# Kernel tuning notes

Measured on AMD Instinct MI355X. Metric: run time of the kernel, lower is better.

The kernel has to match this reference:

```python
import jax, jax.numpy as jnp
import numpy as np

B, I, H = 32768, 128, 128


def setup_inputs() -> dict:
    key = jax.random.key(0)
    ks = jax.random.split(key, 11)
    s = 1.0 / np.sqrt(H)
    return {
        "x": jax.random.normal(ks[0], (B, I), jnp.float32),
        "h": jax.random.normal(ks[1], (B, H), jnp.float32),
        "c": jax.random.normal(ks[2], (B, H), jnp.float32),
        "W1": jax.random.normal(ks[3], (H, I + H), jnp.float32) * s,
        "b1": jax.random.normal(ks[4], (H,), jnp.float32) * s + 1.0,  # forget-gate bias offset 1.0
        "W2": jax.random.normal(ks[5], (H, I + H), jnp.float32) * s,
        "b2": jax.random.normal(ks[6], (H,), jnp.float32) * s,
        "Wf": jax.random.normal(ks[7], (H, I + H), jnp.float32) * s,
        "bf": jax.random.normal(ks[8], (H,), jnp.float32) * s,
        "W3": jax.random.normal(ks[9], (H, I + H), jnp.float32) * s,
        "b3": jax.random.normal(ks[10], (H,), jnp.float32) * s,
    }


def reference(x, h, c, W1, b1, W2, b2, Wf, bf, W3, b3):
    # total_in = inp + hidden (coordinate-list concat == feature concat)
    total = jnp.concatenate([x, h], axis=-1)  # [B, I+H]
    sig1 = jax.nn.sigmoid(total @ W1.T + b1)  # forget gate (bias offset +1)
    sig2 = jax.nn.sigmoid(total @ W2.T + b2)  # input gate
    f_l = jnp.tanh(total @ Wf.T + bf)         # candidate via symmetric f
    sig3 = jax.nn.sigmoid(total @ W3.T + b3)  # output gate
    new_c = c * sig1 + sig2 * f_l             # fused elementwise combine
    new_h = jnp.tanh(new_c) * sig3
    return new_h, new_c
```

## Files before the change

### kernel.cpp

```cpp
#include <hip/hip_runtime.h>

#define B_TOTAL 32768
#define NROWB   128
#define TILE    16
#define NT      8

typedef __attribute__((ext_vector_type(8)))  short    bf16x8;
typedef __attribute__((ext_vector_type(4)))  float    f32x4;
typedef __attribute__((ext_vector_type(2)))  unsigned u32x2;
typedef __attribute__((ext_vector_type(4)))  unsigned u32x4;

__device__ __forceinline__ unsigned rne1(float f) {
    unsigned u = __builtin_bit_cast(unsigned, f);
    return (u + 0x7FFFu + ((u >> 16) & 1u)) >> 16;
}
__device__ __forceinline__ unsigned cvtpk(float lo, float hi) {
    unsigned r;
    asm("v_cvt_pk_bf16_f32 %0, %1, %2" : "=v"(r) : "v"(lo), "v"(hi));
    return r;
}
__device__ __forceinline__ float fsig(float v) {
    return __fdividef(1.0f, 1.0f + __expf(-v));
}
__device__ __forceinline__ float ftanh(float v) {
    return 1.0f - __fdividef(2.0f, 1.0f + __expf(2.0f * v));
}

__global__ void wconv_kernel(const float* __restrict__ w1, const float* __restrict__ w2,
                             const float* __restrict__ wf, const float* __restrict__ w3,
                             u32x4* __restrict__ out) {
    int T = blockIdx.x * 256 + threadIdx.x;
    int F = T >> 6, l = T & 63;
    int s = F >> 4, tau = (F >> 3) & 1, ks = F & 7;
    int n16 = l & 15;
    int g = n16 & 3, hl = n16 >> 2;
    const float* W = (g == 0) ? w1 : (g == 1) ? w2 : (g == 2) ? wf : w3;
    const float* src = W + (s * 8 + tau * 4 + hl) * 256 + ks * 32 + (l >> 4) * 8;
    f32x4 lo = *(const f32x4*)src;
    f32x4 hi = *(const f32x4*)(src + 4);
    u32x4 r;
    r[0] = rne1(lo[0]) | (rne1(lo[1]) << 16);
    r[1] = rne1(lo[2]) | (rne1(lo[3]) << 16);
    r[2] = rne1(hi[0]) | (rne1(hi[1]) << 16);
    r[3] = rne1(hi[2]) | (rne1(hi[3]) << 16);
    out[T] = r;
}

__global__ __launch_bounds__(1024, 4) void lstm_kernel(
    const float* __restrict__ x, const float* __restrict__ h, const float* __restrict__ c,
    const bf16x8* __restrict__ wfrag,
    const float* __restrict__ b1, const float* __restrict__ b2,
    const float* __restrict__ bfv, const float* __restrict__ b3,
    float* __restrict__ out)
{
    __shared__ __align__(16) char smem[2][8192];

    const int tid  = threadIdx.x;
    const int wave = tid >> 6;
    const int lane = tid & 63;
    const int rb   = lane & 15;
    const int c4   = lane >> 4;
    const long row0 = (long)blockIdx.x * NROWB;
    const int col0 = wave * 8 + c4;
    const int col1 = col0 + 4;

    const int ksst  = lane & 7;
    const int chunk = lane >> 3;
    const int k0    = ksst * 32 + chunk * 4;
    const int stoff = ksst * 1024
        + (((((chunk >> 1) << 4) | wave) + ksst) & 63) * 16
        + (chunk & 1) * 8;

    f32x4 ar;
    auto A_ISSUE = [&](int t) {
        const float* base = (k0 < 128)
            ? (x + (row0 + (long)t * TILE + wave) * 128 + k0)
            : (h + (row0 + (long)t * TILE + wave) * 128 + (k0 - 128));
        ar = *(const f32x4*)base;
    };
    auto A_STORE = [&](int b) {
        u32x2 w;
        w[0] = cvtpk(ar[0], ar[1]);
        w[1] = cvtpk(ar[2], ar[3]);
        *(u32x2*)(smem[b & 1] + stoff) = w;
    };

    A_ISSUE(0);

    bf16x8 wfr[2][8];
#pragma unroll
    for (int tau = 0; tau < 2; ++tau)
#pragma unroll
        for (int ks = 0; ks < 8; ++ks)
            wfr[tau][ks] = wfrag[(size_t)((wave * 2 + tau) * 8 + ks) * 64 + lane];

    const f32x4 bias0 = (f32x4){ b1[col0], b2[col0], bfv[col0], b3[col0] };
    const f32x4 bias1 = (f32x4){ b1[col1], b2[col1], bfv[col1], b3[col1] };

    A_STORE(0);
    A_ISSUE(1);

    float cv0 = c[(row0 + rb) * 128 + col0];
    float cv1 = c[(row0 + rb) * 128 + col1];

    float* out_h = out;
    float* out_c = out + (size_t)B_TOTAL * 128;

#pragma unroll 1
    for (int t = 0; t < NT; ++t) {
        asm volatile("s_waitcnt lgkmcnt(0)" ::: "memory");
        __builtin_amdgcn_s_barrier();
        __builtin_amdgcn_sched_barrier(0);

        const char* buf = smem[t & 1];
        const long gr0 = row0 + (long)t * TILE;

        f32x4 acc0 = bias0, acc1 = bias1;

#pragma unroll
        for (int ks = 0; ks < 8; ++ks) {
            bf16x8 af = *(const bf16x8*)(buf + ks * 1024 + ((lane + ks) & 63) * 16);
            acc0 = __builtin_amdgcn_mfma_f32_16x16x32_bf16(wfr[0][ks], af, acc0, 0, 0, 0);
            acc1 = __builtin_amdgcn_mfma_f32_16x16x32_bf16(wfr[1][ks], af, acc1, 0, 0, 0);
        }

        if (t + 1 < NT) {
            A_STORE(t + 1);
            if (t + 2 < NT) A_ISSUE(t + 2);
        }

        const int tn = (t + 1 < NT) ? (t + 1) : (NT - 1);
        const float ncv0 = c[(row0 + (long)tn * TILE + rb) * 128 + col0];
        const float ncv1 = c[(row0 + (long)tn * TILE + rb) * 128 + col1];

        const long orow = (gr0 + rb) * 128;
        {
            const float G1 = fsig(acc0[0]);
            const float G2 = fsig(acc0[1]);
            const float GF = ftanh(acc0[2]);
            const float G3 = fsig(acc0[3]);
            const float nc = cv0 * G1 + G2 * GF;
            out_h[orow + col0] = ftanh(nc) * G3;
            out_c[orow + col0] = nc;
        }
        {
            const float G1 = fsig(acc1[0]);
            const float G2 = fsig(acc1[1]);
            const float GF = ftanh(acc1[2]);
            const float G3 = fsig(acc1[3]);
            const float nc = cv1 * G1 + G2 * GF;
            out_h[orow + col1] = ftanh(nc) * G3;
            out_c[orow + col1] = nc;
        }

        cv0 = ncv0;
        cv1 = ncv1;
    }
}

extern "C" void kernel_launch(void* const* d_in, const int* in_sizes, int n_in,
                              void* d_out, int out_size, void* d_ws, size_t ws_size,
                              hipStream_t stream) {
    (void)in_sizes; (void)n_in; (void)out_size; (void)ws_size;
    const float* x  = (const float*)d_in[0];
    const float* h  = (const float*)d_in[1];
    const float* c  = (const float*)d_in[2];
    const float* W1 = (const float*)d_in[3];
    const float* b1 = (const float*)d_in[4];
    const float* W2 = (const float*)d_in[5];
    const float* b2 = (const float*)d_in[6];
    const float* Wf = (const float*)d_in[7];
    const float* bf = (const float*)d_in[8];
    const float* W3 = (const float*)d_in[9];
    const float* b3 = (const float*)d_in[10];

    wconv_kernel<<<64, 256, 0, stream>>>(W1, W2, Wf, W3, (u32x4*)d_ws);
    lstm_kernel<<<B_TOTAL / NROWB, 1024, 0, stream>>>(
        x, h, c, (const bf16x8*)d_ws, b1, b2, bf, b3, (float*)d_out);
}
```

Baseline: 38.40 us.

## Split hidden columns across block pairs and double the row tile per wave

The kernel now uses 512-thread blocks, each handling half of the hidden columns (column group chosen by block parity), with twice as many blocks launched. Each wave processes 32-row tiles (two 16-row MFMA tiles) over 4 iterations, reusing its weight fragments across both row tiles. A tiles are staged with wider 16-byte LDS stores in two phases interleaved with compute, and setprio is raised around the MFMA loop. The cost is that x/h are read and converted twice (once per column-group block), and c is now loaded directly in the epilogue rather than prefetched.

```diff
diff --git a/kernel.cpp b/kernel.cpp
--- a/kernel.cpp
+++ b/kernel.cpp
@@ -2,12 +2,11 @@
 
 #define B_TOTAL 32768
 #define NROWB   128
-#define TILE    16
-#define NT      8
+#define TILE    32
+#define NT      4
 
 typedef __attribute__((ext_vector_type(8)))  short    bf16x8;
 typedef __attribute__((ext_vector_type(4)))  float    f32x4;
-typedef __attribute__((ext_vector_type(2)))  unsigned u32x2;
 typedef __attribute__((ext_vector_type(4)))  unsigned u32x4;
 
 __device__ __forceinline__ unsigned rne1(float f) {
@@ -46,62 +45,68 @@
     out[T] = r;
 }
 
-__global__ __launch_bounds__(1024, 4) void lstm_kernel(
+__global__ __launch_bounds__(512, 4) void lstm_kernel(
     const float* __restrict__ x, const float* __restrict__ h, const float* __restrict__ c,
     const bf16x8* __restrict__ wfrag,
     const float* __restrict__ b1, const float* __restrict__ b2,
     const float* __restrict__ bfv, const float* __restrict__ b3,
     float* __restrict__ out)
 {
-    __shared__ __align__(16) char smem[2][8192];
+    __shared__ __align__(16) char smem[2][16384];
 
     const int tid  = threadIdx.x;
     const int wave = tid >> 6;
     const int lane = tid & 63;
     const int rb   = lane & 15;
     const int c4   = lane >> 4;
-    const long row0 = (long)blockIdx.x * NROWB;
-    const int col0 = wave * 8 + c4;
+    const int cg   = blockIdx.x & 1;
+    const long row0 = (long)(blockIdx.x >> 1) * NROWB;
+    const int s    = cg * 8 + wave;
+    const int col0 = s * 8 + c4;
     const int col1 = col0 + 4;
 
-    const int ksst  = lane & 7;
-    const int chunk = lane >> 3;
-    const int k0    = ksst * 32 + chunk * 4;
-    const int stoff = ksst * 1024
-        + (((((chunk >> 1) << 4) | wave) + ksst) & 63) * 16
-        + (chunk & 1) * 8;
+    const int srow = tid >> 4;
+    const int seg  = tid & 15;
+    const int sks  = seg >> 1;
+    const int smt  = srow >> 4;
+    const int sr   = srow & 15;
+    const int subA = (seg & 1) * 2;
+    const int offA = sks * 2048 + smt * 1024 + (((subA * 16 + sr) + sks) & 63) * 16;
+    const int offB = sks * 2048 + smt * 1024 + ((((subA + 1) * 16 + sr) + sks) & 63) * 16;
+    const float* const srcbase = (seg < 8) ? x : h;
+    const int koff = (seg < 8) ? seg * 16 : seg * 16 - 128;
 
-    f32x4 ar;
-    auto A_ISSUE = [&](int t) {
-        const float* base = (k0 < 128)
-            ? (x + (row0 + (long)t * TILE + wave) * 128 + k0)
-            : (h + (row0 + (long)t * TILE + wave) * 128 + (k0 - 128));
-        ar = *(const f32x4*)base;
+    f32x4 ar0, ar1;
+    auto ISSUE = [&](int t, int ph) {
+        const float* p = srcbase + (row0 + (long)t * TILE + srow) * 128 + koff + ph * 8;
+        ar0 = *(const f32x4*)(p);
+        ar1 = *(const f32x4*)(p + 4);
     };
-    auto A_STORE = [&](int b) {
-        u32x2 w;
-        w[0] = cvtpk(ar[0], ar[1]);
-        w[1] = cvtpk(ar[2], ar[3]);
-        *(u32x2*)(smem[b & 1] + stoff) = w;
+    auto STORE = [&](int b, int ph) {
+        u32x4 w;
+        w[0] = cvtpk(ar0[0], ar0[1]);
+        w[1] = cvtpk(ar0[2], ar0[3]);
+        w[2] = cvtpk(ar1[0], ar1[1]);
+        w[3] = cvtpk(ar1[2], ar1[3]);
+        *(u32x4*)(smem[b & 1] + (ph ? offB : offA)) = w;
     };
 
-    A_ISSUE(0);
+    ISSUE(0, 0);
 
     bf16x8 wfr[2][8];
 #pragma unroll
     for (int tau = 0; tau < 2; ++tau)
 #pragma unroll
         for (int ks = 0; ks < 8; ++ks)
-            wfr[tau][ks] = wfrag[(size_t)((wave * 2 + tau) * 8 + ks) * 64 + lane];
+            wfr[tau][ks] = wfrag[(size_t)((s * 2 + tau) * 8 + ks) * 64 + lane];
+
+    STORE(0, 0);
+    ISSUE(0, 1);
 
     const f32x4 bias0 = (f32x4){ b1[col0], b2[col0], bfv[col0], b3[col0] };
     const f32x4 bias1 = (f32x4){ b1[col1], b2[col1], bfv[col1], b3[col1] };
 
-    A_STORE(0);
-    A_ISSUE(1);
-
-    float cv0 = c[(row0 + rb) * 128 + col0];
-    float cv1 = c[(row0 + rb) * 128 + col1];
+    STORE(0, 1);
 
     float* out_h = out;
     float* out_c = out + (size_t)B_TOTAL * 128;
@@ -115,46 +120,57 @@
         const char* buf = smem[t & 1];
         const long gr0 = row0 + (long)t * TILE;
 
-        f32x4 acc0 = bias0, acc1 = bias1;
+        if (t + 1 < NT) ISSUE(t + 1, 0);
+
+        f32x4 a00 = bias0, a01 = bias1;
+        f32x4 a10 = bias0, a11 = bias1;
+
+        __builtin_amdgcn_s_setprio(1);
+#pragma unroll
+        for (int ks = 0; ks < 8; ++ks) {
+            const int rot = ((lane + ks) & 63) * 16;
+            bf16x8 af0 = *(const bf16x8*)(buf + ks * 2048 + rot);
+            bf16x8 af1 = *(const bf16x8*)(buf + ks * 2048 + 1024 + rot);
+            a00 = __builtin_amdgcn_mfma_f32_16x16x32_bf16(wfr[0][ks], af0, a00, 0, 0, 0);
+            a01 = __builtin_amdgcn_mfma_f32_16x16x32_bf16(wfr[1][ks], af0, a01, 0, 0, 0);
+            a10 = __builtin_amdgcn_mfma_f32_16x16x32_bf16(wfr[0][ks], af1, a10, 0, 0, 0);
+            a11 = __builtin_amdgcn_mfma_f32_16x16x32_bf16(wfr[1][ks], af1, a11, 0, 0, 0);
+        }
+        __builtin_amdgcn_s_setprio(0);
+
+        if (t + 1 < NT) {
+            STORE(t + 1, 0);
+            ISSUE(t + 1, 1);
+        }
 
 #pragma unroll
-        for (int ks = 0; ks < 8; ++ks) {
-            bf16x8 af = *(const bf16x8*)(buf + ks * 1024 + ((lane + ks) & 63) * 16);
-            acc0 = __builtin_amdgcn_mfma_f32_16x16x32_bf16(wfr[0][ks], af, acc0, 0, 0, 0);
-            acc1 = __builtin_amdgcn_mfma_f32_16x16x32_bf16(wfr[1][ks], af, acc1, 0, 0, 0);
+        for (int mt = 0; mt < 2; ++mt) {
+            const long orow = (gr0 + mt * 16 + rb) * 128;
+            const f32x4 acc0 = mt ? a10 : a00;
+            const f32x4 acc1 = mt ? a11 : a01;
+            const float cva = c[orow + col0];
+            const float cvb = c[orow + col1];
+            {
+                const float G1 = fsig(acc0[0]);
+                const float G2 = fsig(acc0[1]);
+                const float GF = ftanh(acc0[2]);
+                const float G3 = fsig(acc0[3]);
+                const float nc = cva * G1 + G2 * GF;
+                out_h[orow + col0] = ftanh(nc) * G3;
+                out_c[orow + col0] = nc;
+            }
+            {
+                const float G1 = fsig(acc1[0]);
+                const float G2 = fsig(acc1[1]);
+                const float GF = ftanh(acc1[2]);
+                const float G3 = fsig(acc1[3]);
+                const float nc = cvb * G1 + G2 * GF;
+                out_h[orow + col1] = ftanh(nc) * G3;
+                out_c[orow + col1] = nc;
+            }
         }
 
-        if (t + 1 < NT) {
-            A_STORE(t + 1);
-            if (t + 2 < NT) A_ISSUE(t + 2);
-        }
-
-        const int tn = (t + 1 < NT) ? (t + 1) : (NT - 1);
-        const float ncv0 = c[(row0 + (long)tn * TILE + rb) * 128 + col0];
-        const float ncv1 = c[(row0 + (long)tn * TILE + rb) * 128 + col1];
-
-        const long orow = (gr0 + rb) * 128;
-        {
-            const float G1 = fsig(acc0[0]);
-            const float G2 = fsig(acc0[1]);
-            const float GF = ftanh(acc0[2]);
-            const float G3 = fsig(acc0[3]);
-            const float nc = cv0 * G1 + G2 * GF;
-            out_h[orow + col0] = ftanh(nc) * G3;
-            out_c[orow + col0] = nc;
-        }
-        {
-            const float G1 = fsig(acc1[0]);
-            const float G2 = fsig(acc1[1]);
-            const float GF = ftanh(acc1[2]);
-            const float G3 = fsig(acc1[3]);
-            const float nc = cv1 * G1 + G2 * GF;
-            out_h[orow + col1] = ftanh(nc) * G3;
-            out_c[orow + col1] = nc;
-        }
-
-        cv0 = ncv0;
-        cv1 = ncv1;
+        if (t + 1 < NT) STORE(t + 1, 1);
     }
 }
 
@@ -175,6 +191,6 @@
     const float* b3 = (const float*)d_in[10];
 
     wconv_kernel<<<64, 256, 0, stream>>>(W1, W2, Wf, W3, (u32x4*)d_ws);
-    lstm_kernel<<<B_TOTAL / NROWB, 1024, 0, stream>>>(
+    lstm_kernel<<<B_TOTAL / NROWB * 2, 512, 0, stream>>>(
         x, h, c, (const bf16x8*)d_ws, b1, b2, bf, b3, (float*)d_out);
 }
```

Result: slower. 41.59 us (+8.3%).
